# Optimization experiments

Hardware: AMD Instinct MI355X
Metric: run time of the kernel (lower is better)

## Reference

```python
import jax, jax.numpy as jnp
import numpy as np

M, A, H = 1024, 32, 384          # molecules, atoms per molecule, hidden size
ATOM_FDIM, BOND_FDIM = 139, 150  # chemprop featurizer dims (bond feats include src atom feats)
DEPTH = 4
MAX_NB = 4                       # max incoming bonds per atom (ring + skip-ring topology)


def _build_graph():
    # Per-molecule template: ring bonds (i, i+1) and skip bonds (i, i+2) -> degree 4.
    src = np.arange(A)
    E = np.concatenate([np.stack([src, (src + 1) % A], 1),
                        np.stack([src, (src + 2) % A], 1)], 0)  # [2A, 2] undirected (a1, a2)
    nb = E.shape[0]          # undirected bonds per molecule (= 2A)
    db = 2 * nb              # directed bonds per molecule (= 4A)
    # bond 2j originates at a1 (incoming to a2); bond 2j+1 originates at a2 (incoming to a1)
    b2a_t = np.empty(db, np.int64)
    b2a_t[0::2] = E[:, 0]
    b2a_t[1::2] = E[:, 1]
    b2revb_t = np.empty(db, np.int64)
    b2revb_t[0::2] = 2 * np.arange(nb) + 1
    b2revb_t[1::2] = 2 * np.arange(nb)
    a2b_t = [[] for _ in range(A)]
    for j, (a1, a2) in enumerate(E):
        a2b_t[a2].append(2 * j)
        a2b_t[a1].append(2 * j + 1)
    a2b_t = np.asarray(a2b_t, np.int64)  # [A, MAX_NB], every atom has exactly 4 incoming bonds
    mo = np.arange(M)
    # global indices are offset by 1 (index 0 is the BatchMolGraph zero-padding entry)
    a2b = np.concatenate([np.zeros((1, MAX_NB), np.int64),
                          (a2b_t[None] + 1 + db * mo[:, None, None]).reshape(-1, MAX_NB)], 0)
    b2a = np.concatenate([np.zeros(1, np.int64),
                          (b2a_t[None] + 1 + A * mo[:, None]).reshape(-1)], 0)
    b2revb = np.concatenate([np.zeros(1, np.int64),
                             (b2revb_t[None] + 1 + db * mo[:, None]).reshape(-1)], 0)
    return jnp.asarray(a2b), jnp.asarray(b2a), jnp.asarray(b2revb)


def setup_inputs() -> dict:
    key = jax.random.key(0)
    ks = jax.random.split(key, 7)
    n_atoms = 1 + M * A
    n_bonds = 1 + M * 4 * A
    a2b, b2a, b2revb = _build_graph()
    f_atoms = jax.random.normal(ks[0], (n_atoms, ATOM_FDIM), jnp.float32).at[0].set(0.0)
    f_bonds = jax.random.normal(ks[1], (n_bonds, BOND_FDIM), jnp.float32).at[0].set(0.0)
    s = jnp.float32(0.05)
    return {
        'f_atoms': f_atoms,
        'f_bonds': f_bonds,
        'W_i': jax.random.normal(ks[2], (BOND_FDIM, H), jnp.float32) * s,
        'W_h': jax.random.normal(ks[3], (DEPTH - 1, H, H), jnp.float32) * s,  # diff_depth_weights
        'W_o': jax.random.normal(ks[4], (ATOM_FDIM + H, H), jnp.float32) * s,
        'b_o': jnp.zeros((H,), jnp.float32),
        'W_a': jax.random.normal(ks[5], (H, H), jnp.float32) * s,
        'W_b': jax.random.normal(ks[6], (H, H), jnp.float32) * s,
        'b_b': jnp.zeros((H,), jnp.float32),
        'a2b': a2b,
        'b2a': b2a,
        'b2revb': b2revb,
    }


def reference(f_atoms, f_bonds, W_i, W_h, W_o, b_o, W_a, W_b, b_b, a2b, b2a, b2revb):
    # Directed MPNN (Chemprop/SAMPN), dropout=0, no layer norm, normalize_messages=False.
    inp = f_bonds @ W_i                     # [n_bonds, H]
    message = jax.nn.relu(inp)
    for d in range(DEPTH - 1):
        a_msg = message[a2b].sum(axis=1)    # gather incoming bond messages, sum -> [n_atoms, H]
        # m(b: a1->a2) = sum_incoming(a1) - rev_message(b)
        message = jax.nn.relu(inp + (a_msg[b2a] - message[b2revb]) @ W_h[d])
    a_msg = message[a2b].sum(axis=1)        # [n_atoms, H]
    atom_h = jax.nn.relu(jnp.concatenate([f_atoms, a_msg], axis=1) @ W_o + b_o)  # [n_atoms, H]
    # Readout with self-attention per molecule; drop padding row, equal-size molecules.
    cur = atom_h[1:].reshape(M, A, H)
    att = jax.nn.softmax(jnp.einsum('mah,mbh->mab', cur @ W_a, cur), axis=-1)
    att_h = jax.nn.relu(jnp.einsum('mab,mbh->mah', att, cur) @ W_b + b_b)
    return (cur + att_h).sum(axis=1)        # sumstyle readout -> [M, H]
```

## Files before the change

kernel.cpp:

```cpp
#include <hip/hip_runtime.h>
#include <cstdint>
#include <cstddef>


typedef float  floatx4  __attribute__((ext_vector_type(4)));
typedef short  bf16x8   __attribute__((ext_vector_type(8)));
typedef unsigned short ushort_t;
typedef unsigned short ushortx8 __attribute__((ext_vector_type(8)));

#define DEV __device__ __forceinline__

DEV float bf2f(ushort_t u) {
  union { unsigned int i; float f; } v; v.i = ((unsigned int)u) << 16; return v.f;
}
DEV ushort_t f2bf(float f) {
  union { float f; unsigned int i; } v; v.f = f;
  unsigned int r = v.i + 0x7FFFu + ((v.i >> 16) & 1u);
  return (ushort_t)(r >> 16);
}

#define GLD16(gp, lp)                                                          \
  __builtin_amdgcn_global_load_lds(                                            \
      (const __attribute__((address_space(1))) void*)(gp),                     \
      (__attribute__((address_space(3))) void*)(lp), 16, 0, 0)

__global__ void k_conv_fa(const float* __restrict__ fa, ushort_t* __restrict__ cath) {
  int cid = blockIdx.x * 256 + threadIdx.x;
  if (cid >= 32768 * 24) return;
  int a = cid / 24 + 1, j = cid % 24;
  int chunk = (j < 18) ? j : (48 + j);
  const float* s = fa + (size_t)a * 139;
  ushortx8 o;
#pragma unroll
  for (int e = 0; e < 8; e++) { int col = chunk * 8 + e; o[e] = (col < 139) ? f2bf(s[col]) : (ushort_t)0; }
  *(ushortx8*)(cath + (size_t)a * 576 + chunk * 8) = o;
}

__global__ void k_conv_wt(const float* __restrict__ Wi, const float* __restrict__ Wh,
                          const float* __restrict__ Wa, const float* __restrict__ Wb,
                          const float* __restrict__ Wo,
                          ushort_t* __restrict__ wti, ushort_t* __restrict__ wthx,
                          ushort_t* __restrict__ wta, ushort_t* __restrict__ wtb,
                          ushort_t* __restrict__ wto) {
  int cid = blockIdx.x * 256 + threadIdx.x;
  if (cid < 9216) {
    int n = cid / 24, kc = cid % 24; ushortx8 o;
#pragma unroll
    for (int e = 0; e < 8; e++) { int k = kc * 8 + e; o[e] = (k < 150) ? f2bf(Wi[(size_t)k * 384 + n]) : (ushort_t)0; }
    *(ushortx8*)(wti + (size_t)n * 192 + kc * 8) = o; return;
  }
  cid -= 9216;
  if (cid < 82944) {
    int np = cid / 72, kc = cid % 72;
    int d = np / 384, n = np % 384; ushortx8 o;
#pragma unroll
    for (int e = 0; e < 8; e++) {
      float v = 0.f;
      if (kc < 48) { int k = kc * 8 + e; v = Wh[(size_t)d * 147456 + (size_t)k * 384 + n]; }
      else { int k2 = (kc - 48) * 8 + e; v = (k2 < 150) ? Wi[(size_t)k2 * 384 + n] : 0.f; }
      o[e] = f2bf(v);
    }
    *(ushortx8*)(wthx + (size_t)np * 576 + kc * 8) = o; return;
  }
  cid -= 82944;
  if (cid < 18432) {
    int n = cid / 48, kc = cid % 48; ushortx8 o;
#pragma unroll
    for (int e = 0; e < 8; e++) { int k = kc * 8 + e; o[e] = f2bf(Wa[(size_t)k * 384 + n]); }
    *(ushortx8*)(wta + (size_t)n * 384 + kc * 8) = o; return;
  }
  cid -= 18432;
  if (cid < 18432) {
    int n = cid / 48, kc = cid % 48; ushortx8 o;
#pragma unroll
    for (int e = 0; e < 8; e++) { int k = kc * 8 + e; o[e] = f2bf(Wb[(size_t)k * 384 + n]); }
    *(ushortx8*)(wtb + (size_t)n * 384 + kc * 8) = o; return;
  }
  cid -= 18432;
  if (cid < 27648) {
    int n = cid / 72, kc = cid % 72; ushortx8 o;
#pragma unroll
    for (int e = 0; e < 8; e++) {
      int k = kc * 8 + e; float v = 0.f;
      if (k < 139) v = Wo[(size_t)k * 384 + n];
      else if (k >= 144 && k < 528) v = Wo[(size_t)(k - 5) * 384 + n];
      o[e] = f2bf(v);
    }
    *(ushortx8*)(wto + (size_t)n * 576 + kc * 8) = o; return;
  }
}

__global__ __launch_bounds__(512, 4) void k_gemm(
    const ushort_t* __restrict__ A1, int lda1, int K1,
    const float* __restrict__ Af32, int ldaf, int K2,
    const ushort_t* __restrict__ Bt, int ldb,
    ushort_t* __restrict__ Cb, float* __restrict__ Cf,
    const float* __restrict__ bias, int relu)
{
  __shared__ ushort_t LS[448 * 64] __attribute__((aligned(16)));
  const int tid = threadIdx.x;
  const int w = tid >> 6, l = tid & 63;
  const int m0 = blockIdx.x << 6;
  const int lr = l & 15, quad = l >> 4;
  const int NI = (K1 + K2) >> 6;

  floatx4 acc[4][3] = {};

  const int srow8 = l >> 3;
  const int skc   = (l & 7) ^ srow8;

  auto stage = [&](int k0) {
#pragma unroll
    for (int g = 0; g < 7; g++) {
      const int sg = w + (g << 3);
      const int r  = (sg << 3) + srow8;
      ushort_t* lp = LS + ((size_t)sg << 9);
      const int kk = k0 + (skc << 3);
      if (r < 64) {
        if (kk < K1) {
          GLD16(A1 + (size_t)(m0 + r) * lda1 + kk, lp);
        } else {
          const float* src = Af32 + (size_t)(m0 + r) * ldaf;
          ushortx8 o;
#pragma unroll
          for (int e = 0; e < 8; e++) {
            int col = kk - K1 + e;
            int ci  = (col < ldaf) ? col : 0;
            float v = src[ci];
            o[e] = (col < ldaf) ? f2bf(v) : (ushort_t)0;
          }
          *(ushortx8*)(lp + ((size_t)l << 3)) = o;
        }
      } else {
        GLD16(Bt + (size_t)(r - 64) * ldb + kk, lp);
      }
    }
  };

  const int rsw = (lr & 7);
  stage(0);
  for (int i = 0; i < NI; i++) {
    __syncthreads();
    bf16x8 af[4], bf[3];
#pragma unroll
    for (int mt = 0; mt < 4; mt++) {
      int R = (mt << 4) + lr;
      af[mt] = *(const bf16x8*)(LS + (size_t)R * 64 + ((quad ^ rsw) << 3));
    }
#pragma unroll
    for (int nt = 0; nt < 3; nt++) {
      int R = 64 + w * 48 + (nt << 4) + lr;
      bf[nt] = *(const bf16x8*)(LS + (size_t)R * 64 + ((quad ^ rsw) << 3));
    }
#pragma unroll
    for (int mt = 0; mt < 4; mt++)
#pragma unroll
      for (int nt = 0; nt < 3; nt++)
        acc[mt][nt] = __builtin_amdgcn_mfma_f32_16x16x32_bf16(af[mt], bf[nt], acc[mt][nt], 0, 0, 0);
#pragma unroll
    for (int mt = 0; mt < 4; mt++) {
      int R = (mt << 4) + lr;
      af[mt] = *(const bf16x8*)(LS + (size_t)R * 64 + (((4 + quad) ^ rsw) << 3));
    }
#pragma unroll
    for (int nt = 0; nt < 3; nt++) {
      int R = 64 + w * 48 + (nt << 4) + lr;
      bf[nt] = *(const bf16x8*)(LS + (size_t)R * 64 + (((4 + quad) ^ rsw) << 3));
    }
    __syncthreads();
    if (i + 1 < NI) stage((i + 1) << 6);
#pragma unroll
    for (int mt = 0; mt < 4; mt++)
#pragma unroll
      for (int nt = 0; nt < 3; nt++)
        acc[mt][nt] = __builtin_amdgcn_mfma_f32_16x16x32_bf16(af[mt], bf[nt], acc[mt][nt], 0, 0, 0);
  }

#pragma unroll
  for (int mt = 0; mt < 4; mt++) {
#pragma unroll
    for (int nt = 0; nt < 3; nt++) {
      int colg = w * 48 + (nt << 4) + lr;
      float bv = bias ? bias[colg] : 0.f;
#pragma unroll
      for (int r = 0; r < 4; r++) {
        int rowg = m0 + (mt << 4) + (quad << 2) + r;
        size_t off = (size_t)rowg * 384 + colg;
        float v = acc[mt][nt][r] + bv;
        if (relu) v = fmaxf(v, 0.f);
        if (Cf) Cf[off] = v;
        else    Cb[off] = f2bf(v);
      }
    }
  }
}

__global__ void k_fuse(const ushort_t* __restrict__ msrc, const int* __restrict__ a2b,
                       ushort_t* __restrict__ mdst) {
  int cid = blockIdx.x * 256 + threadIdx.x;
  if (cid >= 32768 * 48) return;
  int a = (cid / 48) + 1, c = cid % 48;
  const int4 nb = *(const int4*)(a2b + (size_t)a * 4);
  ushortx8 x0 = *(const ushortx8*)(msrc + (size_t)nb.x * 384 + c * 8);
  ushortx8 x1 = *(const ushortx8*)(msrc + (size_t)nb.y * 384 + c * 8);
  ushortx8 x2 = *(const ushortx8*)(msrc + (size_t)nb.z * 384 + c * 8);
  ushortx8 x3 = *(const ushortx8*)(msrc + (size_t)nb.w * 384 + c * 8);
  float s[8];
#pragma unroll
  for (int e = 0; e < 8; e++)
    s[e] = bf2f(x0[e]) + bf2f(x1[e]) + bf2f(x2[e]) + bf2f(x3[e]);
  int r0 = ((nb.x - 1) ^ 1) + 1;
  int r1 = ((nb.y - 1) ^ 1) + 1;
  int r2 = ((nb.z - 1) ^ 1) + 1;
  int r3 = ((nb.w - 1) ^ 1) + 1;
  ushortx8 o0, o1, o2, o3;
#pragma unroll
  for (int e = 0; e < 8; e++) {
    o0[e] = f2bf(s[e] - bf2f(x0[e]));
    o1[e] = f2bf(s[e] - bf2f(x1[e]));
    o2[e] = f2bf(s[e] - bf2f(x2[e]));
    o3[e] = f2bf(s[e] - bf2f(x3[e]));
  }
  *(ushortx8*)(mdst + (size_t)r0 * 384 + c * 8) = o0;
  *(ushortx8*)(mdst + (size_t)r1 * 384 + c * 8) = o1;
  *(ushortx8*)(mdst + (size_t)r2 * 384 + c * 8) = o2;
  *(ushortx8*)(mdst + (size_t)r3 * 384 + c * 8) = o3;
}

__global__ void k_amsg_cat(const ushort_t* __restrict__ msg, const int* __restrict__ a2b,
                           ushort_t* __restrict__ cath) {
  int cid = blockIdx.x * 256 + threadIdx.x;
  if (cid >= 32768 * 48) return;
  int a = (cid / 48) + 1, c = cid % 48;
  const int4 nb = *(const int4*)(a2b + (size_t)a * 4);
  ushortx8 x0 = *(const ushortx8*)(msg + (size_t)nb.x * 384 + c * 8);
  ushortx8 x1 = *(const ushortx8*)(msg + (size_t)nb.y * 384 + c * 8);
  ushortx8 x2 = *(const ushortx8*)(msg + (size_t)nb.z * 384 + c * 8);
  ushortx8 x3 = *(const ushortx8*)(msg + (size_t)nb.w * 384 + c * 8);
  ushortx8 o;
#pragma unroll
  for (int e = 0; e < 8; e++)
    o[e] = f2bf(bf2f(x0[e]) + bf2f(x1[e]) + bf2f(x2[e]) + bf2f(x3[e]));
  *(ushortx8*)(cath + (size_t)a * 576 + 144 + c * 8) = o;
}

__global__ __launch_bounds__(256) void k_attn(const float* __restrict__ q32,
                                              const ushort_t* __restrict__ cur16,
                                              ushort_t* __restrict__ z16) {
  __shared__ ushort_t cs[32 * 392] __attribute__((aligned(16)));
  __shared__ float sc[32 * 33];
  const int tid = threadIdx.x;
  const size_t base = (size_t)blockIdx.x * 12288;
#pragma unroll
  for (int i = 0; i < 6; i++) {
    int cc = tid + i * 256;
    int row = cc / 48, c = cc % 48;
    *(ushortx8*)(cs + row * 392 + c * 8) = *(const ushortx8*)(cur16 + base + (size_t)cc * 8);
  }
  __syncthreads();
#pragma unroll
  for (int i = 0; i < 4; i++) {
    int p = tid + i * 256;
    int a = p >> 5, b = p & 31;
    const float* qrow = q32 + base + (size_t)a * 384;
    float s = 0.f;
    for (int kc = 0; kc < 48; kc++) {
      const float4* qp = (const float4*)(qrow + kc * 8);
      float4 qa = qp[0], qb = qp[1];
      ushortx8 cv = *(const ushortx8*)(cs + b * 392 + kc * 8);
      s += qa.x * bf2f(cv[0]) + qa.y * bf2f(cv[1]) + qa.z * bf2f(cv[2]) + qa.w * bf2f(cv[3])
         + qb.x * bf2f(cv[4]) + qb.y * bf2f(cv[5]) + qb.z * bf2f(cv[6]) + qb.w * bf2f(cv[7]);
    }
    sc[a * 33 + b] = s;
  }
  __syncthreads();
  if (tid < 32) {
    float mx = -1e30f;
    for (int b = 0; b < 32; b++) mx = fmaxf(mx, sc[tid * 33 + b]);
    float sum = 0.f; float ex[32];
    for (int b = 0; b < 32; b++) { float e = __expf(sc[tid * 33 + b] - mx); ex[b] = e; sum += e; }
    float inv = 1.f / sum;
    for (int b = 0; b < 32; b++) sc[tid * 33 + b] = ex[b] * inv;
  }
  __syncthreads();
#pragma unroll
  for (int i = 0; i < 6; i++) {
    int cc = tid + i * 256;
    int a = cc / 48, hc = cc % 48;
    float acc8[8] = {};
    for (int b = 0; b < 32; b++) {
      float wgt = sc[a * 33 + b];
      ushortx8 cv = *(const ushortx8*)(cs + b * 392 + hc * 8);
#pragma unroll
      for (int e = 0; e < 8; e++) acc8[e] += wgt * bf2f(cv[e]);
    }
    ushortx8 o;
#pragma unroll
    for (int e = 0; e < 8; e++) o[e] = f2bf(acc8[e]);
    *(ushortx8*)(z16 + base + (size_t)cc * 8) = o;
  }
}

__global__ void k_final(const ushort_t* __restrict__ cur16, const ushort_t* __restrict__ r16,
                        float* __restrict__ out) {
  int cid = blockIdx.x * 256 + threadIdx.x;
  if (cid >= 1024 * 48) return;
  int m = cid / 48, hc = cid % 48;
  float acc8[8] = {};
  size_t rb = (size_t)m * 12288 + hc * 8;
  for (int a = 0; a < 32; a++) {
    ushortx8 cu = *(const ushortx8*)(cur16 + rb + (size_t)a * 384);
    ushortx8 rr = *(const ushortx8*)(r16 + rb + (size_t)a * 384);
#pragma unroll
    for (int e = 0; e < 8; e++) acc8[e] += bf2f(cu[e]) + bf2f(rr[e]);
  }
  float* o = out + (size_t)m * 384 + hc * 8;
#pragma unroll
  for (int e = 0; e < 8; e++) o[e] = acc8[e];
}

extern "C" void kernel_launch(void* const* d_in, const int* in_sizes, int n_in,
                              void* d_out, int out_size, void* d_ws, size_t ws_size,
                              hipStream_t stream) {
  (void)in_sizes; (void)n_in; (void)out_size;
  const float* f_atoms = (const float*)d_in[0];
  const float* f_bonds = (const float*)d_in[1];
  const float* W_i = (const float*)d_in[2];
  const float* W_h = (const float*)d_in[3];
  const float* W_o = (const float*)d_in[4];
  const float* b_o = (const float*)d_in[5];
  const float* W_a = (const float*)d_in[6];
  const float* W_b = (const float*)d_in[7];
  const float* b_b = (const float*)d_in[8];
  const int* a2b = (const int*)d_in[9];
  const int* b2a = (const int*)d_in[10];
  const int* b2revb = (const int*)d_in[11];
  (void)b2a; (void)b2revb;
  float* out = (float*)d_out;

  char* ws = (char*)d_ws;
  size_t off = 0;
  auto alloc = [&](size_t bytes) -> char* {
    char* p = ws + off; off += (bytes + 255) & ~(size_t)255; return p;
  };
  ushort_t* msg0 = (ushort_t*)alloc(131073ull * 384 * 2);
  ushort_t* msg1 = (ushort_t*)alloc(131073ull * 384 * 2);
  ushort_t* wti  = (ushort_t*)alloc(384ull * 192 * 2);
  ushort_t* wthx = (ushort_t*)alloc(3ull * 384 * 576 * 2);
  ushort_t* wta  = (ushort_t*)alloc(384ull * 384 * 2);
  ushort_t* wtb  = (ushort_t*)alloc(384ull * 384 * 2);
  ushort_t* wto  = (ushort_t*)alloc(384ull * 576 * 2);
  if (ws_size < off) return;

  ushort_t* cath  = (ushort_t*)msg0;
  ushort_t* cur16 = (ushort_t*)((char*)msg0 + 37749888);
  float*    q32 = (float*)msg1;
  ushort_t* z16 = (ushort_t*)((char*)msg1 + 50331648);
  ushort_t* r16 = (ushort_t*)((char*)msg1 + 75497472);

  k_conv_wt<<<612, 256, 0, stream>>>(W_i, W_h, W_a, W_b, W_o, wti, wthx, wta, wtb, wto);

  k_gemm<<<2048, 512, 0, stream>>>(nullptr, 0, 0,
                                   f_bonds + 150, 150, 192,
                                   wti, 192, msg0 + 384, nullptr, nullptr, 1);

  ushort_t* mcur = msg0;
  ushort_t* mnxt = msg1;
  for (int d = 0; d < 3; d++) {
    k_fuse<<<6144, 256, 0, stream>>>(mcur, a2b, mnxt);
    k_gemm<<<2048, 512, 0, stream>>>(mnxt + 384, 384, 384,
                                     f_bonds + 150, 150, 192,
                                     wthx + (size_t)d * 221184, 576,
                                     mnxt + 384, nullptr, nullptr, 1);
    ushort_t* t = mcur; mcur = mnxt; mnxt = t;
  }
  k_amsg_cat<<<6144, 256, 0, stream>>>(mcur, a2b, cath);
  k_conv_fa<<<3072, 256, 0, stream>>>(f_atoms, cath);
  k_gemm<<<512, 512, 0, stream>>>(cath + 576, 576, 576,
                                  nullptr, 0, 0,
                                  wto, 576, cur16, nullptr, b_o, 1);
  k_gemm<<<512, 512, 0, stream>>>(cur16, 384, 384,
                                  nullptr, 0, 0,
                                  wta, 384, nullptr, q32, nullptr, 0);
  k_attn<<<1024, 256, 0, stream>>>(q32, cur16, z16);
  k_gemm<<<512, 512, 0, stream>>>(z16, 384, 384,
                                  nullptr, 0, 0,
                                  wtb, 384, r16, nullptr, b_b, 1);
  k_final<<<192, 256, 0, stream>>>(cur16, r16, out);
}
```

Baseline: 804.1 us.

## Pre-convert bond features to bf16 and make message fuse in-place per molecule

```diff
diff --git a/kernel.cpp b/kernel.cpp
--- a/kernel.cpp
+++ b/kernel.cpp
@@ -23,6 +23,17 @@
   __builtin_amdgcn_global_load_lds(                                            \
       (const __attribute__((address_space(1))) void*)(gp),                     \
       (__attribute__((address_space(3))) void*)(lp), 16, 0, 0)
+
+__global__ void k_conv_fb(const float* __restrict__ fb, ushort_t* __restrict__ dst) {
+  int cid = blockIdx.x * 256 + threadIdx.x;
+  if (cid >= 131073 * 24) return;
+  int row = cid / 24, j = cid % 24;
+  const float* s = fb + (size_t)row * 150;
+  ushortx8 o;
+#pragma unroll
+  for (int e = 0; e < 8; e++) { int col = j * 8 + e; o[e] = (col < 150) ? f2bf(s[col]) : (ushort_t)0; }
+  *(ushortx8*)(dst + (size_t)row * 192 + j * 8) = o;
+}
 
 __global__ void k_conv_fa(const float* __restrict__ fa, ushort_t* __restrict__ cath) {
   int cid = blockIdx.x * 256 + threadIdx.x;
@@ -92,7 +103,7 @@
 
 __global__ __launch_bounds__(512, 4) void k_gemm(
     const ushort_t* __restrict__ A1, int lda1, int K1,
-    const float* __restrict__ Af32, int ldaf, int K2,
+    const ushort_t* __restrict__ A2, int lda2, int K2,
     const ushort_t* __restrict__ Bt, int ldb,
     ushort_t* __restrict__ Cb, float* __restrict__ Cf,
     const float* __restrict__ bias, int relu)
@@ -117,20 +128,8 @@
       ushort_t* lp = LS + ((size_t)sg << 9);
       const int kk = k0 + (skc << 3);
       if (r < 64) {
-        if (kk < K1) {
-          GLD16(A1 + (size_t)(m0 + r) * lda1 + kk, lp);
-        } else {
-          const float* src = Af32 + (size_t)(m0 + r) * ldaf;
-          ushortx8 o;
-#pragma unroll
-          for (int e = 0; e < 8; e++) {
-            int col = kk - K1 + e;
-            int ci  = (col < ldaf) ? col : 0;
-            float v = src[ci];
-            o[e] = (col < ldaf) ? f2bf(v) : (ushort_t)0;
-          }
-          *(ushortx8*)(lp + ((size_t)l << 3)) = o;
-        }
+        if (kk < K1) GLD16(A1 + (size_t)(m0 + r) * lda1 + kk, lp);
+        else         GLD16(A2 + (size_t)(m0 + r) * lda2 + (kk - K1), lp);
       } else {
         GLD16(Bt + (size_t)(r - 64) * ldb + kk, lp);
       }
@@ -195,36 +194,51 @@
   }
 }
 
-__global__ void k_fuse(const ushort_t* __restrict__ msrc, const int* __restrict__ a2b,
-                       ushort_t* __restrict__ mdst) {
-  int cid = blockIdx.x * 256 + threadIdx.x;
-  if (cid >= 32768 * 48) return;
-  int a = (cid / 48) + 1, c = cid % 48;
-  const int4 nb = *(const int4*)(a2b + (size_t)a * 4);
-  ushortx8 x0 = *(const ushortx8*)(msrc + (size_t)nb.x * 384 + c * 8);
-  ushortx8 x1 = *(const ushortx8*)(msrc + (size_t)nb.y * 384 + c * 8);
-  ushortx8 x2 = *(const ushortx8*)(msrc + (size_t)nb.z * 384 + c * 8);
-  ushortx8 x3 = *(const ushortx8*)(msrc + (size_t)nb.w * 384 + c * 8);
-  float s[8];
-#pragma unroll
-  for (int e = 0; e < 8; e++)
-    s[e] = bf2f(x0[e]) + bf2f(x1[e]) + bf2f(x2[e]) + bf2f(x3[e]);
-  int r0 = ((nb.x - 1) ^ 1) + 1;
-  int r1 = ((nb.y - 1) ^ 1) + 1;
-  int r2 = ((nb.z - 1) ^ 1) + 1;
-  int r3 = ((nb.w - 1) ^ 1) + 1;
-  ushortx8 o0, o1, o2, o3;
-#pragma unroll
-  for (int e = 0; e < 8; e++) {
-    o0[e] = f2bf(s[e] - bf2f(x0[e]));
-    o1[e] = f2bf(s[e] - bf2f(x1[e]));
-    o2[e] = f2bf(s[e] - bf2f(x2[e]));
-    o3[e] = f2bf(s[e] - bf2f(x3[e]));
-  }
-  *(ushortx8*)(mdst + (size_t)r0 * 384 + c * 8) = o0;
-  *(ushortx8*)(mdst + (size_t)r1 * 384 + c * 8) = o1;
-  *(ushortx8*)(mdst + (size_t)r2 * 384 + c * 8) = o2;
-  *(ushortx8*)(mdst + (size_t)r3 * 384 + c * 8) = o3;
+__global__ __launch_bounds__(512) void k_fuse(ushort_t* __restrict__ msg,
+                                              const int* __restrict__ a2b) {
+  const int m = blockIdx.x;
+  const int tid = threadIdx.x;
+  ushortx8 x0[3], x1[3], x2[3], x3[3];
+  int4 nbs[3];
+  int cs[3];
+#pragma unroll
+  for (int it = 0; it < 3; it++) {
+    int i  = tid + (it << 9);
+    int al = i / 48, c = i % 48;
+    int a  = 1 + (m << 5) + al;
+    int4 nb = *(const int4*)(a2b + (size_t)a * 4);
+    nbs[it] = nb; cs[it] = c;
+    x0[it] = *(const ushortx8*)(msg + (size_t)nb.x * 384 + c * 8);
+    x1[it] = *(const ushortx8*)(msg + (size_t)nb.y * 384 + c * 8);
+    x2[it] = *(const ushortx8*)(msg + (size_t)nb.z * 384 + c * 8);
+    x3[it] = *(const ushortx8*)(msg + (size_t)nb.w * 384 + c * 8);
+  }
+  __syncthreads();
+#pragma unroll
+  for (int it = 0; it < 3; it++) {
+    const int4 nb = nbs[it];
+    const int c = cs[it];
+    float s[8];
+#pragma unroll
+    for (int e = 0; e < 8; e++)
+      s[e] = bf2f(x0[it][e]) + bf2f(x1[it][e]) + bf2f(x2[it][e]) + bf2f(x3[it][e]);
+    int r0 = ((nb.x - 1) ^ 1) + 1;
+    int r1 = ((nb.y - 1) ^ 1) + 1;
+    int r2 = ((nb.z - 1) ^ 1) + 1;
+    int r3 = ((nb.w - 1) ^ 1) + 1;
+    ushortx8 o0, o1, o2, o3;
+#pragma unroll
+    for (int e = 0; e < 8; e++) {
+      o0[e] = f2bf(s[e] - bf2f(x0[it][e]));
+      o1[e] = f2bf(s[e] - bf2f(x1[it][e]));
+      o2[e] = f2bf(s[e] - bf2f(x2[it][e]));
+      o3[e] = f2bf(s[e] - bf2f(x3[it][e]));
+    }
+    *(ushortx8*)(msg + (size_t)r0 * 384 + c * 8) = o0;
+    *(ushortx8*)(msg + (size_t)r1 * 384 + c * 8) = o1;
+    *(ushortx8*)(msg + (size_t)r2 * 384 + c * 8) = o2;
+    *(ushortx8*)(msg + (size_t)r3 * 384 + c * 8) = o3;
+  }
 }
 
 __global__ void k_amsg_cat(const ushort_t* __restrict__ msg, const int* __restrict__ a2b,
@@ -343,8 +357,8 @@
   auto alloc = [&](size_t bytes) -> char* {
     char* p = ws + off; off += (bytes + 255) & ~(size_t)255; return p;
   };
-  ushort_t* msg0 = (ushort_t*)alloc(131073ull * 384 * 2);
-  ushort_t* msg1 = (ushort_t*)alloc(131073ull * 384 * 2);
+  char* R1 = alloc(131073ull * 384 * 2);
+  char* R2 = alloc(62915712);
   ushort_t* wti  = (ushort_t*)alloc(384ull * 192 * 2);
   ushort_t* wthx = (ushort_t*)alloc(3ull * 384 * 576 * 2);
   ushort_t* wta  = (ushort_t*)alloc(384ull * 384 * 2);
@@ -352,39 +366,34 @@
   ushort_t* wto  = (ushort_t*)alloc(384ull * 576 * 2);
   if (ws_size < off) return;
 
-  ushort_t* cath  = (ushort_t*)msg0;
-  ushort_t* cur16 = (ushort_t*)((char*)msg0 + 37749888);
-  float*    q32 = (float*)msg1;
-  ushort_t* z16 = (ushort_t*)((char*)msg1 + 50331648);
-  ushort_t* r16 = (ushort_t*)((char*)msg1 + 75497472);
-
+  ushort_t* msg   = (ushort_t*)R1;
+  float*    q32   = (float*)R1;
+  ushort_t* z16   = (ushort_t*)(R1 + 50331648);
+  ushort_t* r16   = (ushort_t*)(R1 + 75497472);
+  ushort_t* fb192 = (ushort_t*)R2;
+  ushort_t* cath  = (ushort_t*)R2;
+  ushort_t* cur16 = (ushort_t*)(R2 + 37749888);
+
+  k_conv_fb<<<12289, 256, 0, stream>>>(f_bonds, fb192);
   k_conv_wt<<<612, 256, 0, stream>>>(W_i, W_h, W_a, W_b, W_o, wti, wthx, wta, wtb, wto);
 
-  k_gemm<<<2048, 512, 0, stream>>>(nullptr, 0, 0,
-                                   f_bonds + 150, 150, 192,
-                                   wti, 192, msg0 + 384, nullptr, nullptr, 1);
-
-  ushort_t* mcur = msg0;
-  ushort_t* mnxt = msg1;
+  k_gemm<<<2048, 512, 0, stream>>>(nullptr, 0, 0, fb192 + 192, 192, 192,
+                                   wti, 192, msg + 384, nullptr, nullptr, 1);
+
   for (int d = 0; d < 3; d++) {
-    k_fuse<<<6144, 256, 0, stream>>>(mcur, a2b, mnxt);
-    k_gemm<<<2048, 512, 0, stream>>>(mnxt + 384, 384, 384,
-                                     f_bonds + 150, 150, 192,
+    k_fuse<<<1024, 512, 0, stream>>>(msg, a2b);
+    k_gemm<<<2048, 512, 0, stream>>>(msg + 384, 384, 384, fb192 + 192, 192, 192,
                                      wthx + (size_t)d * 221184, 576,
-                                     mnxt + 384, nullptr, nullptr, 1);
-    ushort_t* t = mcur; mcur = mnxt; mnxt = t;
-  }
-  k_amsg_cat<<<6144, 256, 0, stream>>>(mcur, a2b, cath);
+                                     msg + 384, nullptr, nullptr, 1);
+  }
+  k_amsg_cat<<<6144, 256, 0, stream>>>(msg, a2b, cath);
   k_conv_fa<<<3072, 256, 0, stream>>>(f_atoms, cath);
-  k_gemm<<<512, 512, 0, stream>>>(cath + 576, 576, 576,
-                                  nullptr, 0, 0,
+  k_gemm<<<512, 512, 0, stream>>>(cath + 576, 576, 576, nullptr, 0, 0,
                                   wto, 576, cur16, nullptr, b_o, 1);
-  k_gemm<<<512, 512, 0, stream>>>(cur16, 384, 384,
-                                  nullptr, 0, 0,
+  k_gemm<<<512, 512, 0, stream>>>(cur16, 384, 384, nullptr, 0, 0,
                                   wta, 384, nullptr, q32, nullptr, 0);
   k_attn<<<1024, 256, 0, stream>>>(q32, cur16, z16);
-  k_gemm<<<512, 512, 0, stream>>>(z16, 384, 384,
-                                  nullptr, 0, 0,
+  k_gemm<<<512, 512, 0, stream>>>(z16, 384, 384, nullptr, 0, 0,
                                   wtb, 384, r16, nullptr, b_b, 1);
   k_final<<<192, 256, 0, stream>>>(cur16, r16, out);
 }
```

After: 702.2 us. 12.7% less time.
